# Kernel optimization log

Measured on AMD Instinct MI355X. Metric: run time of the kernel, lower is better.

## Reference

```python
import jax, jax.numpy as jnp
import numpy as np

B, S, H = 32, 512, 768
VOCAB, MAX_POS, TYPE_VOCAB = 30522, 512, 2
N_COLS, MAX_HLEN = 32, 16
EPS = 1e-12


def setup_inputs() -> dict:
    key = jax.random.key(0)
    ks = jax.random.split(key, 16)
    input_ids = jax.random.randint(ks[0], (B, S), 0, VOCAB)
    header_ids = jax.random.randint(ks[1], (B, N_COLS, MAX_HLEN), 0, VOCAB)
    token_type_ids = jax.random.randint(ks[2], (B, S), 0, TYPE_VOCAB)
    match_type_ids = jax.random.randint(ks[3], (B, S), 0, 11)
    type_idx = jax.random.randint(ks[4], (B, S), 0, 6)
    # distinct scatter positions per batch row (the original dict keys ki are unique)
    col_pos = jnp.sort(jnp.argsort(jax.random.uniform(ks[5], (B, S)), axis=1)[:, :N_COLS], axis=1)
    col_idx = jax.random.randint(ks[6], (B, N_COLS), 0, N_COLS)
    header_len = jax.random.randint(ks[7], (B, N_COLS), 0, MAX_HLEN + 1)  # 0 -> skip
    word_emb = jax.random.normal(ks[8], (VOCAB, H), dtype=jnp.float32) * 0.02
    pos_emb = jax.random.normal(ks[9], (MAX_POS, H), dtype=jnp.float32) * 0.02
    tok_type_emb = jax.random.normal(ks[10], (TYPE_VOCAB, H), dtype=jnp.float32) * 0.02
    match_emb = jax.random.normal(ks[11], (11, H), dtype=jnp.float32) * 0.02
    type_emb = jax.random.normal(ks[12], (6, H), dtype=jnp.float32) * 0.02
    ln_w = jnp.ones((H,), dtype=jnp.float32)
    ln_b = jnp.zeros((H,), dtype=jnp.float32)
    return {"input_ids": input_ids, "header_ids": header_ids,
            "token_type_ids": token_type_ids, "match_type_ids": match_type_ids,
            "type_idx": type_idx, "col_pos": col_pos, "col_idx": col_idx,
            "header_len": header_len, "word_emb": word_emb, "pos_emb": pos_emb,
            "tok_type_emb": tok_type_emb, "match_emb": match_emb,
            "type_emb": type_emb, "ln_w": ln_w, "ln_b": ln_b}


def reference(input_ids, header_ids, token_type_ids, match_type_ids, type_idx,
              col_pos, col_idx, header_len, word_emb, pos_emb, tok_type_emb,
              match_emb, type_emb, ln_w, ln_b):
    b, s = input_ids.shape
    words = word_emb[input_ids]                    # [B,S,H]
    header = word_emb[header_ids]                  # [B,C,L,H]
    L = header_ids.shape[2]
    # variable-length mean pool over header tokens
    mask = (jnp.arange(L)[None, None, :] < header_len[:, :, None]).astype(words.dtype)
    denom = jnp.maximum(header_len, 1).astype(words.dtype)[..., None]
    pooled = jnp.einsum('bclh,bcl->bch', header, mask) / denom   # [B,C,H]
    # scatter pooled column embeddings into word embeddings at col_pos (skip len==0)
    b_idx = jnp.arange(b)[:, None]
    sel = pooled[b_idx, col_idx]                   # [B,C,H]
    valid = (header_len[b_idx, col_idx] > 0)[..., None]
    cur = words[b_idx, col_pos]
    words = words.at[b_idx, col_pos].set(jnp.where(valid, sel, cur))
    emb = (words
           + pos_emb[jnp.arange(s)][None, :, :]
           + tok_type_emb[token_type_ids]
           + match_emb[match_type_ids]
           + type_emb[type_idx])
    # TF-style LayerNorm (eps inside sqrt)
    u = emb.mean(-1, keepdims=True)
    var = jnp.square(emb - u).mean(-1, keepdims=True)
    x = (emb - u) / jnp.sqrt(var + EPS)
    return ln_w * x + ln_b
```

## Files before the change

kernel.cpp:

```cpp
#include <hip/hip_runtime.h>

#define B_ 32
#define S_ 512
#define H_ 768
#define C_ 32
#define L_ 16
#define VOCAB_ 30522

typedef float f4 __attribute__((ext_vector_type(4)));

__device__ __forceinline__ f4 ld4(const float* p) {
    return *reinterpret_cast<const f4*>(p);
}

__global__ __launch_bounds__(256) void pool_kernel(
    const int* __restrict__ header_ids,
    const int* __restrict__ header_len,
    const float* __restrict__ word_emb,
    float* __restrict__ pooled)
{
    const int wi   = blockIdx.x * 4 + (threadIdx.x >> 6);
    const int lane = threadIdx.x & 63;
    const int hlen = header_len[wi];
    if (hlen <= 0) return;

    const int h = lane << 2;
    const int* hid = header_ids + wi * L_;
    f4 a0 = {0,0,0,0}, a1 = {0,0,0,0}, a2 = {0,0,0,0};
    for (int l = 0; l < hlen; ++l) {
        const float* r = word_emb + (size_t)hid[l] * H_ + h;
        a0 += ld4(r);
        a1 += ld4(r + 256);
        a2 += ld4(r + 512);
    }
    const float inv = 1.0f / (float)hlen;
    float* o = pooled + (size_t)wi * H_ + h;
    *reinterpret_cast<f4*>(o)       = a0 * inv;
    *reinterpret_cast<f4*>(o + 256) = a1 * inv;
    *reinterpret_cast<f4*>(o + 512) = a2 * inv;
}

__global__ __launch_bounds__(256) void bert_emb_kernel(
    const int* __restrict__ input_ids,
    const int* __restrict__ token_type_ids,
    const int* __restrict__ match_type_ids,
    const int* __restrict__ type_idx,
    const int* __restrict__ col_pos,
    const int* __restrict__ col_idx,
    const int* __restrict__ header_len,
    const float* __restrict__ word_emb,
    const float* __restrict__ pos_emb,
    const float* __restrict__ tok_type_emb,
    const float* __restrict__ match_emb,
    const float* __restrict__ type_emb,
    const float* __restrict__ ln_w,
    const float* __restrict__ ln_b,
    const float* __restrict__ pooled,
    float* __restrict__ out)
{
    const int tok  = blockIdx.x * 4 + (threadIdx.x >> 6);
    const int lane = threadIdx.x & 63;
    const int b    = tok >> 9;
    const int s    = tok & (S_ - 1);

    const int cp = col_pos[(b << 5) + (lane & 31)];
    unsigned long long m = __ballot(cp == s) & 0xffffffffULL;
    const float* wrow;
    if (m) {
        const int cm = __ffsll(m) - 1;
        const int ci = col_idx[(b << 5) + cm];
        if (header_len[(b << 5) + ci] > 0)
            wrow = pooled + (size_t)((b << 5) + ci) * H_;
        else
            wrow = word_emb + (size_t)input_ids[tok] * H_;
    } else {
        wrow = word_emb + (size_t)input_ids[tok] * H_;
    }

    const int h = lane << 2;
    f4 a0 = ld4(wrow + h);
    f4 a1 = ld4(wrow + h + 256);
    f4 a2 = ld4(wrow + h + 512);
    {
        const float* r = pos_emb + s * H_ + h;
        a0 += ld4(r); a1 += ld4(r + 256); a2 += ld4(r + 512);
    }
    {
        const float* r = tok_type_emb + token_type_ids[tok] * H_ + h;
        a0 += ld4(r); a1 += ld4(r + 256); a2 += ld4(r + 512);
    }
    {
        const float* r = match_emb + match_type_ids[tok] * H_ + h;
        a0 += ld4(r); a1 += ld4(r + 256); a2 += ld4(r + 512);
    }
    {
        const float* r = type_emb + type_idx[tok] * H_ + h;
        a0 += ld4(r); a1 += ld4(r + 256); a2 += ld4(r + 512);
    }

    float s1 = a0.x+a0.y+a0.z+a0.w + a1.x+a1.y+a1.z+a1.w + a2.x+a2.y+a2.z+a2.w;
    float s2 = a0.x*a0.x+a0.y*a0.y+a0.z*a0.z+a0.w*a0.w
             + a1.x*a1.x+a1.y*a1.y+a1.z*a1.z+a1.w*a1.w
             + a2.x*a2.x+a2.y*a2.y+a2.z*a2.z+a2.w*a2.w;
    #pragma unroll
    for (int off = 32; off > 0; off >>= 1) {
        s1 += __shfl_xor(s1, off);
        s2 += __shfl_xor(s2, off);
    }
    const float mean = s1 * (1.0f / H_);
    float var = fmaxf(s2 * (1.0f / H_) - mean * mean, 0.0f);
    const float rstd = rsqrtf(var + 1e-12f);

    float* op = out + (size_t)tok * H_ + h;
    {
        f4 w = ld4(ln_w + h), c = ld4(ln_b + h);
        f4 o = (a0 - mean) * rstd * w + c;
        __builtin_nontemporal_store(o, reinterpret_cast<f4*>(op));
    }
    {
        f4 w = ld4(ln_w + h + 256), c = ld4(ln_b + h + 256);
        f4 o = (a1 - mean) * rstd * w + c;
        __builtin_nontemporal_store(o, reinterpret_cast<f4*>(op + 256));
    }
    {
        f4 w = ld4(ln_w + h + 512), c = ld4(ln_b + h + 512);
        f4 o = (a2 - mean) * rstd * w + c;
        __builtin_nontemporal_store(o, reinterpret_cast<f4*>(op + 512));
    }
}

extern "C" void kernel_launch(void* const* d_in, const int* in_sizes, int n_in,
                              void* d_out, int out_size, void* d_ws, size_t ws_size,
                              hipStream_t stream) {
    const int* input_ids      = (const int*)d_in[0];
    const int* header_ids     = (const int*)d_in[1];
    const int* token_type_ids = (const int*)d_in[2];
    const int* match_type_ids = (const int*)d_in[3];
    const int* type_idx       = (const int*)d_in[4];
    const int* col_pos        = (const int*)d_in[5];
    const int* col_idx        = (const int*)d_in[6];
    const int* header_len     = (const int*)d_in[7];
    const float* word_emb     = (const float*)d_in[8];
    const float* pos_emb      = (const float*)d_in[9];
    const float* tok_type_emb = (const float*)d_in[10];
    const float* match_emb    = (const float*)d_in[11];
    const float* type_emb     = (const float*)d_in[12];
    const float* ln_w         = (const float*)d_in[13];
    const float* ln_b         = (const float*)d_in[14];
    float* out    = (float*)d_out;
    float* pooled = (float*)d_ws;

    pool_kernel<<<(B_ * C_) / 4, 256, 0, stream>>>(
        header_ids, header_len, word_emb, pooled);

    bert_emb_kernel<<<(B_ * S_) / 4, 256, 0, stream>>>(
        input_ids, token_type_ids, match_type_ids, type_idx,
        col_pos, col_idx, header_len, word_emb, pos_emb, tok_type_emb,
        match_emb, type_emb, ln_w, ln_b, pooled, out);
}
```

Before: 203.1 us.

## Fuse header mean-pooling into embedding kernel, drop separate pool launch

```diff
diff --git a/kernel.cpp b/kernel.cpp
--- a/kernel.cpp
+++ b/kernel.cpp
@@ -5,7 +5,6 @@
 #define H_ 768
 #define C_ 32
 #define L_ 16
-#define VOCAB_ 30522
 
 typedef float f4 __attribute__((ext_vector_type(4)));
 
@@ -13,35 +12,9 @@
     return *reinterpret_cast<const f4*>(p);
 }
 
-__global__ __launch_bounds__(256) void pool_kernel(
-    const int* __restrict__ header_ids,
-    const int* __restrict__ header_len,
-    const float* __restrict__ word_emb,
-    float* __restrict__ pooled)
-{
-    const int wi   = blockIdx.x * 4 + (threadIdx.x >> 6);
-    const int lane = threadIdx.x & 63;
-    const int hlen = header_len[wi];
-    if (hlen <= 0) return;
-
-    const int h = lane << 2;
-    const int* hid = header_ids + wi * L_;
-    f4 a0 = {0,0,0,0}, a1 = {0,0,0,0}, a2 = {0,0,0,0};
-    for (int l = 0; l < hlen; ++l) {
-        const float* r = word_emb + (size_t)hid[l] * H_ + h;
-        a0 += ld4(r);
-        a1 += ld4(r + 256);
-        a2 += ld4(r + 512);
-    }
-    const float inv = 1.0f / (float)hlen;
-    float* o = pooled + (size_t)wi * H_ + h;
-    *reinterpret_cast<f4*>(o)       = a0 * inv;
-    *reinterpret_cast<f4*>(o + 256) = a1 * inv;
-    *reinterpret_cast<f4*>(o + 512) = a2 * inv;
-}
-
 __global__ __launch_bounds__(256) void bert_emb_kernel(
     const int* __restrict__ input_ids,
+    const int* __restrict__ header_ids,
     const int* __restrict__ token_type_ids,
     const int* __restrict__ match_type_ids,
     const int* __restrict__ type_idx,
@@ -55,7 +28,6 @@
     const float* __restrict__ type_emb,
     const float* __restrict__ ln_w,
     const float* __restrict__ ln_b,
-    const float* __restrict__ pooled,
     float* __restrict__ out)
 {
     const int tok  = blockIdx.x * 4 + (threadIdx.x >> 6);
@@ -65,22 +37,31 @@
 
     const int cp = col_pos[(b << 5) + (lane & 31)];
     unsigned long long m = __ballot(cp == s) & 0xffffffffULL;
-    const float* wrow;
+    int use_pool = 0, ci = 0, hlen = 0;
     if (m) {
         const int cm = __ffsll(m) - 1;
-        const int ci = col_idx[(b << 5) + cm];
-        if (header_len[(b << 5) + ci] > 0)
-            wrow = pooled + (size_t)((b << 5) + ci) * H_;
-        else
-            wrow = word_emb + (size_t)input_ids[tok] * H_;
-    } else {
-        wrow = word_emb + (size_t)input_ids[tok] * H_;
+        ci   = col_idx[(b << 5) + cm];
+        hlen = header_len[(b << 5) + ci];
+        use_pool = (hlen > 0);
     }
 
     const int h = lane << 2;
-    f4 a0 = ld4(wrow + h);
-    f4 a1 = ld4(wrow + h + 256);
-    f4 a2 = ld4(wrow + h + 512);
+    f4 a0, a1, a2;
+
+    if (use_pool) {
+        a0 = (f4){0,0,0,0}; a1 = (f4){0,0,0,0}; a2 = (f4){0,0,0,0};
+        const int* hid = header_ids + ((b << 5) + ci) * L_;
+        for (int l = 0; l < hlen; ++l) {
+            const float* r = word_emb + (size_t)hid[l] * H_ + h;
+            a0 += ld4(r); a1 += ld4(r + 256); a2 += ld4(r + 512);
+        }
+        const float inv = 1.0f / (float)hlen;
+        a0 *= inv; a1 *= inv; a2 *= inv;
+    } else {
+        const float* r = word_emb + (size_t)input_ids[tok] * H_ + h;
+        a0 = ld4(r); a1 = ld4(r + 256); a2 = ld4(r + 512);
+    }
+
     {
         const float* r = pos_emb + s * H_ + h;
         a0 += ld4(r); a1 += ld4(r + 256); a2 += ld4(r + 512);
@@ -147,14 +128,10 @@
     const float* type_emb     = (const float*)d_in[12];
     const float* ln_w         = (const float*)d_in[13];
     const float* ln_b         = (const float*)d_in[14];
-    float* out    = (float*)d_out;
-    float* pooled = (float*)d_ws;
-
-    pool_kernel<<<(B_ * C_) / 4, 256, 0, stream>>>(
-        header_ids, header_len, word_emb, pooled);
+    float* out = (float*)d_out;
 
     bert_emb_kernel<<<(B_ * S_) / 4, 256, 0, stream>>>(
-        input_ids, token_type_ids, match_type_ids, type_idx,
+        input_ids, header_ids, token_type_ids, match_type_ids, type_idx,
         col_pos, col_idx, header_len, word_emb, pos_emb, tok_type_emb,
-        match_emb, type_emb, ln_w, ln_b, pooled, out);
+        match_emb, type_emb, ln_w, ln_b, out);
 }
```

New measurement: 191.0 us. 1.06x faster.
